# Optimization experiments

Hardware: AMD Instinct MI355X
Metric: run time of the kernel (lower is better)

The kernel has to match this reference:

```python
import jax, jax.numpy as jnp
import numpy as np

BASE_ALPHA = 0.05
NUM_ITER = 2
EPS = 1e-06


def setup_inputs() -> dict:
    key = jax.random.key(0)
    k1, k2 = jax.random.split(key)
    pred = jax.random.normal(k1, (8, 8192, 3), dtype=jnp.float32)
    partial = jax.random.normal(k2, (8, 2048, 3), dtype=jnp.float32)
    return {"pred": pred, "partial": partial}


def _cdist(a, b):
    # Euclidean pairwise distances via ||a||^2 - 2ab + ||b||^2 (avoids [B,N,M,3] temp).
    a2 = jnp.sum(a * a, axis=-1)  # [B,N]
    b2 = jnp.sum(b * b, axis=-1)  # [B,M]
    d2 = a2[:, :, None] - 2.0 * jnp.einsum('bnd,bmd->bnm', a, b) + b2[:, None, :]
    return jnp.sqrt(jnp.maximum(d2, 0.0))


def reference(pred, partial):
    refined = pred
    for _ in range(NUM_ITER):
        dist = _cdist(refined, partial)          # [B,N,M]
        min_dist = jnp.min(dist, axis=-1)        # [B,N]
        min_idx = jnp.argmin(dist, axis=-1)      # [B,N]
        nearest = jnp.take_along_axis(partial, min_idx[:, :, None], axis=1)  # [B,N,3]
        dist_norm = min_dist / (jnp.max(min_dist, axis=-1, keepdims=True) + EPS)
        alpha = BASE_ALPHA * (2.0 - dist_norm)   # [B,N]
        refined = refined + alpha[:, :, None] * (nearest - refined)
    return refined
```

## Files before the change

### kernel.cpp

```cpp
#include <hip/hip_runtime.h>
#include <math.h>

#define BATCH 8
#define NPRED 8192
#define MPART 2048
#define NPTS  (BATCH * NPRED)
#define MTOT  (BATCH * MPART)
#define QPL   4
#define SPLIT 16
#define PTS_PER_SPLIT (MPART / SPLIT)
#define GPS   (PTS_PER_SPLIT / 4)
#define QPB   256
#define NBLK  (NPTS / QPB)
#define BLK_PER_B (NPRED / QPB)
#define BASE_ALPHA 0.05f
#define EPS 1e-6f

__global__ __launch_bounds__(256) void prep_kernel(const float* __restrict__ partial,
                                                   float* __restrict__ ppgf,
                                                   float4* __restrict__ near4) {
    const int m = blockIdx.x * 256 + threadIdx.x;
    const float* p = partial + 3u * (unsigned)m;
    const float x = p[0], y = p[1], z = p[2];
    const int g = m >> 2, c = m & 3;
    float* base = ppgf + (size_t)g * 16 + c;
    base[0]  = -2.0f * x;
    base[4]  = -2.0f * y;
    base[8]  = -2.0f * z;
    base[12] = fmaf(x, x, fmaf(y, y, z * z));
    near4[m] = make_float4(x, y, z, 0.0f);
}

template <bool FUSE>
__global__ __launch_bounds__(1024) void nn_kernel(
    const float* __restrict__ src,
    const float4* __restrict__ ppg,
    const float4* __restrict__ near4,
    const float* md_in, const int* idx_in,
    const float* __restrict__ bmax_in,
    float* __restrict__ refined_out,
    float* md_out, int* idx_out,
    float* __restrict__ bmax_out)
{
    __shared__ float4 ldsP[2048];
    __shared__ float smax[4];
    unsigned long long* lk = (unsigned long long*)ldsP;

    const int qb   = blockIdx.x;
    const int b    = qb >> 5;
    const int tid  = threadIdx.x;
    const int wave = tid >> 6, lane = tid & 63;
    const int split = wave;

    const float4* gsrc = ppg + ((size_t)b << 11);
    ldsP[tid]        = gsrc[tid];
    ldsP[tid + 1024] = gsrc[tid + 1024];

    float axq[QPL], ayq[QPL], azq[QPL], a2q[QPL];
    if (FUSE) {
        float v = bmax_in[(b << 5) + (lane & 31)];
        #pragma unroll
        for (int o = 32; o > 0; o >>= 1) v = fmaxf(v, __shfl_down(v, o, 64));
        const float maxv = __shfl(v, 0, 64);
        #pragma unroll
        for (int j = 0; j < QPL; ++j) {
            const int t = (qb << 8) + (j << 6) + lane;
            const float md = md_in[t];
            const int   id = idx_in[t];
            const float alpha = BASE_ALPHA * (2.0f - md / (maxv + EPS));
            const float4 nb = near4[((size_t)b << 11) + id];
            const float* p = src + 3u * (unsigned)t;
            const float px = p[0], py = p[1], pz = p[2];
            axq[j] = fmaf(alpha, nb.x - px, px);
            ayq[j] = fmaf(alpha, nb.y - py, py);
            azq[j] = fmaf(alpha, nb.z - pz, pz);
            if (split == 0) {
                float* o = refined_out + 3u * (unsigned)t;
                o[0] = axq[j]; o[1] = ayq[j]; o[2] = azq[j];
            }
        }
    } else {
        #pragma unroll
        for (int j = 0; j < QPL; ++j) {
            const int t = (qb << 8) + (j << 6) + lane;
            const float* p = src + 3u * (unsigned)t;
            axq[j] = p[0]; ayq[j] = p[1]; azq[j] = p[2];
        }
    }
    #pragma unroll
    for (int j = 0; j < QPL; ++j)
        a2q[j] = fmaf(axq[j], axq[j], fmaf(ayq[j], ayq[j], azq[j] * azq[j]));

    __syncthreads();

    const float4* wp = ldsP + split * (GPS * 4);
    float best[QPL]; int bg[QPL];
    #pragma unroll
    for (int j = 0; j < QPL; ++j) { best[j] = 1e30f; bg[j] = 0; }

    #pragma unroll 2
    for (int i = 0; i < GPS; ++i) {
        const float4 X = wp[4 * i + 0];
        const float4 Y = wp[4 * i + 1];
        const float4 Z = wp[4 * i + 2];
        const float4 W = wp[4 * i + 3];
        #pragma unroll
        for (int j = 0; j < QPL; ++j) {
            const float ax = axq[j], ay = ayq[j], az = azq[j];
            const float d0 = fmaf(Z.x, az, fmaf(Y.x, ay, X.x * ax)) + W.x;
            const float d1 = fmaf(Z.y, az, fmaf(Y.y, ay, X.y * ax)) + W.y;
            const float d2 = fmaf(Z.z, az, fmaf(Y.z, ay, X.z * ax)) + W.z;
            const float d3 = fmaf(Z.w, az, fmaf(Y.w, ay, X.w * ax)) + W.w;
            const float gm = fminf(fminf(fminf(d0, d1), d2), d3);
            if (gm < best[j]) bg[j] = i;
            best[j] = fminf(best[j], gm);
        }
    }

    unsigned long long key[QPL];
    #pragma unroll
    for (int j = 0; j < QPL; ++j) {
        const int gi = bg[j];
        const float4 X = wp[4 * gi + 0];
        const float4 Y = wp[4 * gi + 1];
        const float4 Z = wp[4 * gi + 2];
        const float4 W = wp[4 * gi + 3];
        const float ax = axq[j], ay = ayq[j], az = azq[j];
        const float d0 = fmaf(Z.x, az, fmaf(Y.x, ay, X.x * ax)) + W.x;
        const float d1 = fmaf(Z.y, az, fmaf(Y.y, ay, X.y * ax)) + W.y;
        const float d2 = fmaf(Z.z, az, fmaf(Y.z, ay, X.z * ax)) + W.z;
        const float bv = best[j];
        int c;
        if      (d0 == bv) c = 0;
        else if (d1 == bv) c = 1;
        else if (d2 == bv) c = 2;
        else               c = 3;
        const int m = (split << 7) + (gi << 2) + c;
        const float dd = fmaxf(bv + a2q[j], 0.0f);
        key[j] = ((unsigned long long)__float_as_uint(dd) << 32) | (unsigned)m;
    }

    __syncthreads();
    #pragma unroll
    for (int j = 0; j < QPL; ++j)
        lk[split * QPB + (j << 6) + lane] = key[j];
    __syncthreads();

    if (wave < 4) {
        const int q2 = (wave << 6) + lane;
        unsigned long long kk = lk[q2];
        #pragma unroll
        for (int s = 1; s < SPLIT; ++s) {
            const unsigned long long k = lk[s * QPB + q2];
            if (k < kk) kk = k;
        }
        const float md = sqrtf(__uint_as_float((unsigned)(kk >> 32)));
        const int t2 = (qb << 8) + q2;
        md_out[t2]  = md;
        idx_out[t2] = (int)(kk & 0xffffffffu);
        float w = md;
        #pragma unroll
        for (int o = 32; o > 0; o >>= 1) w = fmaxf(w, __shfl_down(w, o, 64));
        if (lane == 0) smax[wave] = w;
    }
    __syncthreads();
    if (tid == 0)
        bmax_out[qb] = fmaxf(fmaxf(smax[0], smax[1]), fmaxf(smax[2], smax[3]));
}

__global__ __launch_bounds__(256) void update_kernel(
    const float* __restrict__ refined1,
    const float4* __restrict__ near4,
    const float* __restrict__ md2,
    const int*   __restrict__ idx2,
    const float* __restrict__ bmax2,
    float* __restrict__ out)
{
    const int t = blockIdx.x * 256 + threadIdx.x;
    const int b = t >> 13;
    const int lane = threadIdx.x & 63;
    float v = bmax2[(b << 5) + (lane & 31)];
    #pragma unroll
    for (int o = 32; o > 0; o >>= 1) v = fmaxf(v, __shfl_down(v, o, 64));
    const float maxv = __shfl(v, 0, 64);
    const float md = md2[t];
    const int   id = idx2[t];
    const float alpha = BASE_ALPHA * (2.0f - md / (maxv + EPS));
    const float4 nb = near4[((size_t)b << 11) + id];
    const float* p = refined1 + 3u * (unsigned)t;
    const float px = p[0], py = p[1], pz = p[2];
    float* o = out + 3u * (unsigned)t;
    o[0] = fmaf(alpha, nb.x - px, px);
    o[1] = fmaf(alpha, nb.y - py, py);
    o[2] = fmaf(alpha, nb.z - pz, pz);
}

extern "C" void kernel_launch(void* const* d_in, const int* in_sizes, int n_in,
                              void* d_out, int out_size, void* d_ws, size_t ws_size,
                              hipStream_t stream) {
    const float* pred    = (const float*)d_in[0];
    const float* partial = (const float*)d_in[1];
    float* out = (float*)d_out;

    char* ws = (char*)d_ws;
    float4* ppg   = (float4*)ws;
    float4* near4 = (float4*)(ws + 262144);
    float*  ref1  = (float*)(ws + 524288);
    float*  md1   = (float*)(ws + 1310720);
    int*    idx1  = (int*)(ws + 1572864);
    float*  bmax1 = (float*)(ws + 1835008);
    float*  bmax2 = bmax1 + NBLK;

    prep_kernel<<<MTOT / 256, 256, 0, stream>>>(partial, (float*)ppg, near4);

    nn_kernel<false><<<NBLK, 1024, 0, stream>>>(
        pred, ppg, near4, nullptr, nullptr, nullptr, nullptr, md1, idx1, bmax1);

    nn_kernel<true><<<NBLK, 1024, 0, stream>>>(
        pred, ppg, near4, md1, idx1, bmax1, ref1, md1, idx1, bmax2);

    update_kernel<<<NPTS / 256, 256, 0, stream>>>(ref1, near4, md1, idx1, bmax2, out);
}
```

Measured before the change: 98.96 us.

## Stream partial-point groups via scalar loads instead of LDS staging

The inner nearest-neighbour loop now reads each group of four precomputed partial points straight from global memory with inline s_load_dwordx16 into scalar registers, using a wave-uniform split index. This drops the LDS staging copy, the barrier that followed it, and the per-lane LDS reads. Each iteration waits on lgkmcnt(0) before computing, so scalar load latency is exposed with little overlap. The final re-check now reads the winning group from global memory.

```diff
diff --git a/kernel.cpp b/kernel.cpp
--- a/kernel.cpp
+++ b/kernel.cpp
@@ -16,6 +16,8 @@
 #define BASE_ALPHA 0.05f
 #define EPS 1e-6f
 
+typedef float fx16 __attribute__((ext_vector_type(16)));
+
 __global__ __launch_bounds__(256) void prep_kernel(const float* __restrict__ partial,
                                                    float* __restrict__ ppgf,
                                                    float4* __restrict__ near4) {
@@ -42,19 +44,14 @@
     float* md_out, int* idx_out,
     float* __restrict__ bmax_out)
 {
-    __shared__ float4 ldsP[2048];
+    __shared__ unsigned long long lk[SPLIT * QPB];
     __shared__ float smax[4];
-    unsigned long long* lk = (unsigned long long*)ldsP;
 
     const int qb   = blockIdx.x;
     const int b    = qb >> 5;
     const int tid  = threadIdx.x;
     const int wave = tid >> 6, lane = tid & 63;
-    const int split = wave;
-
-    const float4* gsrc = ppg + ((size_t)b << 11);
-    ldsP[tid]        = gsrc[tid];
-    ldsP[tid + 1024] = gsrc[tid + 1024];
+    const int split = __builtin_amdgcn_readfirstlane(wave);
 
     float axq[QPL], ayq[QPL], azq[QPL], a2q[QPL];
     if (FUSE) {
@@ -91,40 +88,54 @@
     for (int j = 0; j < QPL; ++j)
         a2q[j] = fmaf(axq[j], axq[j], fmaf(ayq[j], ayq[j], azq[j] * azq[j]));
 
-    __syncthreads();
-
-    const float4* wp = ldsP + split * (GPS * 4);
+    const fx16* gq = (const fx16*)(ppg + ((size_t)b << 11) + ((size_t)split << 7));
+
     float best[QPL]; int bg[QPL];
     #pragma unroll
     for (int j = 0; j < QPL; ++j) { best[j] = 1e30f; bg[j] = 0; }
 
-    #pragma unroll 2
-    for (int i = 0; i < GPS; ++i) {
-        const float4 X = wp[4 * i + 0];
-        const float4 Y = wp[4 * i + 1];
-        const float4 Z = wp[4 * i + 2];
-        const float4 W = wp[4 * i + 3];
+    #pragma unroll 1
+    for (int ii = 0; ii < GPS; ii += 2) {
+        fx16 A, B;
+        asm volatile("s_load_dwordx16 %0, %2, 0\n\t"
+                     "s_load_dwordx16 %1, %2, 64"
+                     : "=&s"(A), "=&s"(B)
+                     : "s"(gq + ii));
+        asm volatile("s_waitcnt lgkmcnt(0)" : "+s"(A), "+s"(B));
+
         #pragma unroll
         for (int j = 0; j < QPL; ++j) {
             const float ax = axq[j], ay = ayq[j], az = azq[j];
-            const float d0 = fmaf(Z.x, az, fmaf(Y.x, ay, X.x * ax)) + W.x;
-            const float d1 = fmaf(Z.y, az, fmaf(Y.y, ay, X.y * ax)) + W.y;
-            const float d2 = fmaf(Z.z, az, fmaf(Y.z, ay, X.z * ax)) + W.z;
-            const float d3 = fmaf(Z.w, az, fmaf(Y.w, ay, X.w * ax)) + W.w;
+            const float d0 = fmaf(A[8],  az, fmaf(A[4], ay, A[0] * ax)) + A[12];
+            const float d1 = fmaf(A[9],  az, fmaf(A[5], ay, A[1] * ax)) + A[13];
+            const float d2 = fmaf(A[10], az, fmaf(A[6], ay, A[2] * ax)) + A[14];
+            const float d3 = fmaf(A[11], az, fmaf(A[7], ay, A[3] * ax)) + A[15];
             const float gm = fminf(fminf(fminf(d0, d1), d2), d3);
-            if (gm < best[j]) bg[j] = i;
+            if (gm < best[j]) bg[j] = ii;
             best[j] = fminf(best[j], gm);
         }
-    }
-
+        #pragma unroll
+        for (int j = 0; j < QPL; ++j) {
+            const float ax = axq[j], ay = ayq[j], az = azq[j];
+            const float d0 = fmaf(B[8],  az, fmaf(B[4], ay, B[0] * ax)) + B[12];
+            const float d1 = fmaf(B[9],  az, fmaf(B[5], ay, B[1] * ax)) + B[13];
+            const float d2 = fmaf(B[10], az, fmaf(B[6], ay, B[2] * ax)) + B[14];
+            const float d3 = fmaf(B[11], az, fmaf(B[7], ay, B[3] * ax)) + B[15];
+            const float gm = fminf(fminf(fminf(d0, d1), d2), d3);
+            if (gm < best[j]) bg[j] = ii + 1;
+            best[j] = fminf(best[j], gm);
+        }
+    }
+
+    const float4* wpg = ppg + ((size_t)b << 11) + ((size_t)split << 7);
     unsigned long long key[QPL];
     #pragma unroll
     for (int j = 0; j < QPL; ++j) {
         const int gi = bg[j];
-        const float4 X = wp[4 * gi + 0];
-        const float4 Y = wp[4 * gi + 1];
-        const float4 Z = wp[4 * gi + 2];
-        const float4 W = wp[4 * gi + 3];
+        const float4 X = wpg[4 * gi + 0];
+        const float4 Y = wpg[4 * gi + 1];
+        const float4 Z = wpg[4 * gi + 2];
+        const float4 W = wpg[4 * gi + 3];
         const float ax = axq[j], ay = ayq[j], az = azq[j];
         const float d0 = fmaf(Z.x, az, fmaf(Y.x, ay, X.x * ax)) + W.x;
         const float d1 = fmaf(Z.y, az, fmaf(Y.y, ay, X.y * ax)) + W.y;
@@ -140,7 +151,6 @@
         key[j] = ((unsigned long long)__float_as_uint(dd) << 32) | (unsigned)m;
     }
 
-    __syncthreads();
     #pragma unroll
     for (int j = 0; j < QPL; ++j)
         lk[split * QPB + (j << 6) + lane] = key[j];
```

Result: slower. 108.7 us (+9.8%).

## Fuse all passes into one cooperative kernel with grid syncs

Applied to the files above, without the earlier changes.

Replaces the prep, two nearest-neighbour passes and the update kernel with a single cooperative kernel. Each block builds its batch's partial-point tile in LDS, and grid.sync is used to exchange the per-block distance maxima between iterations. Per-point state (refined coordinates, min distance, index) stays in registers and LDS instead of round-tripping through global memory, and three launches disappear. The cost is two grid-wide barriers and the requirement that all 256 blocks of 1024 threads be co-resident, which depends on the device's CU count and the larger LDS footprint per block.

```diff
diff --git a/kernel.cpp b/kernel.cpp
--- a/kernel.cpp
+++ b/kernel.cpp
@@ -1,99 +1,36 @@
 #include <hip/hip_runtime.h>
+#include <hip/hip_cooperative_groups.h>
 #include <math.h>
+
+namespace cg = cooperative_groups;
 
 #define BATCH 8
 #define NPRED 8192
 #define MPART 2048
 #define NPTS  (BATCH * NPRED)
-#define MTOT  (BATCH * MPART)
 #define QPL   4
 #define SPLIT 16
 #define PTS_PER_SPLIT (MPART / SPLIT)
 #define GPS   (PTS_PER_SPLIT / 4)
 #define QPB   256
 #define NBLK  (NPTS / QPB)
-#define BLK_PER_B (NPRED / QPB)
 #define BASE_ALPHA 0.05f
 #define EPS 1e-6f
 
-__global__ __launch_bounds__(256) void prep_kernel(const float* __restrict__ partial,
-                                                   float* __restrict__ ppgf,
-                                                   float4* __restrict__ near4) {
-    const int m = blockIdx.x * 256 + threadIdx.x;
-    const float* p = partial + 3u * (unsigned)m;
-    const float x = p[0], y = p[1], z = p[2];
-    const int g = m >> 2, c = m & 3;
-    float* base = ppgf + (size_t)g * 16 + c;
-    base[0]  = -2.0f * x;
-    base[4]  = -2.0f * y;
-    base[8]  = -2.0f * z;
-    base[12] = fmaf(x, x, fmaf(y, y, z * z));
-    near4[m] = make_float4(x, y, z, 0.0f);
-}
-
-template <bool FUSE>
-__global__ __launch_bounds__(1024) void nn_kernel(
-    const float* __restrict__ src,
-    const float4* __restrict__ ppg,
-    const float4* __restrict__ near4,
-    const float* md_in, const int* idx_in,
-    const float* __restrict__ bmax_in,
-    float* __restrict__ refined_out,
-    float* md_out, int* idx_out,
-    float* __restrict__ bmax_out)
+struct SMem {
+    float4 tileP[2048];
+    unsigned long long lk[SPLIT * QPB];
+    float md_s[QPB];
+    int   idx_s[QPB];
+    float smax[4];
+};
+
+__device__ __forceinline__ void nn_pass(
+    SMem& sm, int qb, int tid, int wave, int lane, int split,
+    const float axq[QPL], const float ayq[QPL], const float azq[QPL],
+    const float a2q[QPL], float* __restrict__ bmax_entry)
 {
-    __shared__ float4 ldsP[2048];
-    __shared__ float smax[4];
-    unsigned long long* lk = (unsigned long long*)ldsP;
-
-    const int qb   = blockIdx.x;
-    const int b    = qb >> 5;
-    const int tid  = threadIdx.x;
-    const int wave = tid >> 6, lane = tid & 63;
-    const int split = wave;
-
-    const float4* gsrc = ppg + ((size_t)b << 11);
-    ldsP[tid]        = gsrc[tid];
-    ldsP[tid + 1024] = gsrc[tid + 1024];
-
-    float axq[QPL], ayq[QPL], azq[QPL], a2q[QPL];
-    if (FUSE) {
-        float v = bmax_in[(b << 5) + (lane & 31)];
-        #pragma unroll
-        for (int o = 32; o > 0; o >>= 1) v = fmaxf(v, __shfl_down(v, o, 64));
-        const float maxv = __shfl(v, 0, 64);
-        #pragma unroll
-        for (int j = 0; j < QPL; ++j) {
-            const int t = (qb << 8) + (j << 6) + lane;
-            const float md = md_in[t];
-            const int   id = idx_in[t];
-            const float alpha = BASE_ALPHA * (2.0f - md / (maxv + EPS));
-            const float4 nb = near4[((size_t)b << 11) + id];
-            const float* p = src + 3u * (unsigned)t;
-            const float px = p[0], py = p[1], pz = p[2];
-            axq[j] = fmaf(alpha, nb.x - px, px);
-            ayq[j] = fmaf(alpha, nb.y - py, py);
-            azq[j] = fmaf(alpha, nb.z - pz, pz);
-            if (split == 0) {
-                float* o = refined_out + 3u * (unsigned)t;
-                o[0] = axq[j]; o[1] = ayq[j]; o[2] = azq[j];
-            }
-        }
-    } else {
-        #pragma unroll
-        for (int j = 0; j < QPL; ++j) {
-            const int t = (qb << 8) + (j << 6) + lane;
-            const float* p = src + 3u * (unsigned)t;
-            axq[j] = p[0]; ayq[j] = p[1]; azq[j] = p[2];
-        }
-    }
-    #pragma unroll
-    for (int j = 0; j < QPL; ++j)
-        a2q[j] = fmaf(axq[j], axq[j], fmaf(ayq[j], ayq[j], azq[j] * azq[j]));
-
-    __syncthreads();
-
-    const float4* wp = ldsP + split * (GPS * 4);
+    const float4* wp = sm.tileP + split * (GPS * 4);
     float best[QPL]; int bg[QPL];
     #pragma unroll
     for (int j = 0; j < QPL; ++j) { best[j] = 1e30f; bg[j] = 0; }
@@ -143,56 +80,138 @@
     __syncthreads();
     #pragma unroll
     for (int j = 0; j < QPL; ++j)
-        lk[split * QPB + (j << 6) + lane] = key[j];
+        sm.lk[split * QPB + (j << 6) + lane] = key[j];
     __syncthreads();
 
     if (wave < 4) {
         const int q2 = (wave << 6) + lane;
-        unsigned long long kk = lk[q2];
+        unsigned long long kk = sm.lk[q2];
         #pragma unroll
         for (int s = 1; s < SPLIT; ++s) {
-            const unsigned long long k = lk[s * QPB + q2];
+            const unsigned long long k = sm.lk[s * QPB + q2];
             if (k < kk) kk = k;
         }
         const float md = sqrtf(__uint_as_float((unsigned)(kk >> 32)));
-        const int t2 = (qb << 8) + q2;
-        md_out[t2]  = md;
-        idx_out[t2] = (int)(kk & 0xffffffffu);
+        sm.md_s[q2]  = md;
+        sm.idx_s[q2] = (int)(kk & 0xffffffffu);
         float w = md;
         #pragma unroll
         for (int o = 32; o > 0; o >>= 1) w = fmaxf(w, __shfl_down(w, o, 64));
-        if (lane == 0) smax[wave] = w;
+        if (lane == 0) sm.smax[wave] = w;
     }
     __syncthreads();
     if (tid == 0)
-        bmax_out[qb] = fmaxf(fmaxf(smax[0], smax[1]), fmaxf(smax[2], smax[3]));
+        *bmax_entry = fmaxf(fmaxf(sm.smax[0], sm.smax[1]),
+                            fmaxf(sm.smax[2], sm.smax[3]));
 }
 
-__global__ __launch_bounds__(256) void update_kernel(
-    const float* __restrict__ refined1,
-    const float4* __restrict__ near4,
-    const float* __restrict__ md2,
-    const int*   __restrict__ idx2,
-    const float* __restrict__ bmax2,
-    float* __restrict__ out)
+__global__ void __launch_bounds__(1024) fused_kernel(
+    const float* __restrict__ pred,
+    const float* __restrict__ partial,
+    float* __restrict__ out,
+    float* __restrict__ bmax1,
+    float* __restrict__ bmax2)
 {
-    const int t = blockIdx.x * 256 + threadIdx.x;
-    const int b = t >> 13;
-    const int lane = threadIdx.x & 63;
-    float v = bmax2[(b << 5) + (lane & 31)];
+    __shared__ SMem sm;
+    cg::grid_group grid = cg::this_grid();
+
+    const int qb   = blockIdx.x;
+    const int b    = qb >> 5;
+    const int tid  = threadIdx.x;
+    const int wave = tid >> 6, lane = tid & 63;
+    const int split = wave;
+
+    float axq[QPL], ayq[QPL], azq[QPL], a2q[QPL];
+    #pragma unroll
+    for (int j = 0; j < QPL; ++j) {
+        const int t = (qb << 8) + (j << 6) + lane;
+        const float* p = pred + 3u * (unsigned)t;
+        axq[j] = p[0]; ayq[j] = p[1]; azq[j] = p[2];
+    }
+    #pragma unroll
+    for (int j = 0; j < QPL; ++j)
+        a2q[j] = fmaf(axq[j], axq[j], fmaf(ayq[j], ayq[j], azq[j] * azq[j]));
+
+    {
+        float4* raws = (float4*)sm.lk;
+        const float4* psrc = (const float4*)(partial + (size_t)b * MPART * 3);
+        raws[tid] = psrc[tid];
+        if (tid < 512) raws[tid + 1024] = psrc[tid + 1024];
+    }
+    __syncthreads();
+
+    {
+        const float* rf = (const float*)sm.lk;
+        float* tpf = (float*)sm.tileP;
+        #pragma unroll
+        for (int k = 0; k < 2; ++k) {
+            const int m = tid + k * 1024;
+            const float x = rf[3 * m], y = rf[3 * m + 1], z = rf[3 * m + 2];
+            const int g = m >> 2, c = m & 3;
+            float* basep = tpf + g * 16 + c;
+            basep[0]  = -2.0f * x;
+            basep[4]  = -2.0f * y;
+            basep[8]  = -2.0f * z;
+            basep[12] = fmaf(x, x, fmaf(y, y, z * z));
+        }
+    }
+    __syncthreads();
+
+    nn_pass(sm, qb, tid, wave, lane, split, axq, ayq, azq, a2q, bmax1 + qb);
+    __threadfence();
+    grid.sync();
+
+    float v = bmax1[(b << 5) + (lane & 31)];
     #pragma unroll
     for (int o = 32; o > 0; o >>= 1) v = fmaxf(v, __shfl_down(v, o, 64));
-    const float maxv = __shfl(v, 0, 64);
-    const float md = md2[t];
-    const int   id = idx2[t];
-    const float alpha = BASE_ALPHA * (2.0f - md / (maxv + EPS));
-    const float4 nb = near4[((size_t)b << 11) + id];
-    const float* p = refined1 + 3u * (unsigned)t;
-    const float px = p[0], py = p[1], pz = p[2];
-    float* o = out + 3u * (unsigned)t;
-    o[0] = fmaf(alpha, nb.x - px, px);
-    o[1] = fmaf(alpha, nb.y - py, py);
-    o[2] = fmaf(alpha, nb.z - pz, pz);
+    const float maxv1 = __shfl(v, 0, 64);
+
+    const float* tpf = (const float*)sm.tileP;
+    #pragma unroll
+    for (int j = 0; j < QPL; ++j) {
+        const int q = (j << 6) + lane;
+        const float md = sm.md_s[q];
+        const int  id  = sm.idx_s[q];
+        const float alpha = BASE_ALPHA * (2.0f - md / (maxv1 + EPS));
+        const int g = id >> 2, c = id & 3;
+        const float nbx = -0.5f * tpf[g * 16 + c];
+        const float nby = -0.5f * tpf[g * 16 + 4 + c];
+        const float nbz = -0.5f * tpf[g * 16 + 8 + c];
+        const float px = axq[j], py = ayq[j], pz = azq[j];
+        axq[j] = fmaf(alpha, nbx - px, px);
+        ayq[j] = fmaf(alpha, nby - py, py);
+        azq[j] = fmaf(alpha, nbz - pz, pz);
+    }
+    #pragma unroll
+    for (int j = 0; j < QPL; ++j)
+        a2q[j] = fmaf(axq[j], axq[j], fmaf(ayq[j], ayq[j], azq[j] * azq[j]));
+
+    nn_pass(sm, qb, tid, wave, lane, split, axq, ayq, azq, a2q, bmax2 + qb);
+    __threadfence();
+    grid.sync();
+
+    float v2 = bmax2[(b << 5) + (lane & 31)];
+    #pragma unroll
+    for (int o = 32; o > 0; o >>= 1) v2 = fmaxf(v2, __shfl_down(v2, o, 64));
+    const float maxv2 = __shfl(v2, 0, 64);
+
+    if (wave < 4) {
+        const int j = wave;
+        const int q = (j << 6) + lane;
+        const float md = sm.md_s[q];
+        const int  id  = sm.idx_s[q];
+        const float alpha = BASE_ALPHA * (2.0f - md / (maxv2 + EPS));
+        const int g = id >> 2, c = id & 3;
+        const float nbx = -0.5f * tpf[g * 16 + c];
+        const float nby = -0.5f * tpf[g * 16 + 4 + c];
+        const float nbz = -0.5f * tpf[g * 16 + 8 + c];
+        const float px = axq[j], py = ayq[j], pz = azq[j];
+        const int t = (qb << 8) + q;
+        float* o = out + 3u * (unsigned)t;
+        o[0] = fmaf(alpha, nbx - px, px);
+        o[1] = fmaf(alpha, nby - py, py);
+        o[2] = fmaf(alpha, nbz - pz, pz);
+    }
 }
 
 extern "C" void kernel_launch(void* const* d_in, const int* in_sizes, int n_in,
@@ -203,21 +222,11 @@
     float* out = (float*)d_out;
 
     char* ws = (char*)d_ws;
-    float4* ppg   = (float4*)ws;
-    float4* near4 = (float4*)(ws + 262144);
-    float*  ref1  = (float*)(ws + 524288);
-    float*  md1   = (float*)(ws + 1310720);
-    int*    idx1  = (int*)(ws + 1572864);
-    float*  bmax1 = (float*)(ws + 1835008);
-    float*  bmax2 = bmax1 + NBLK;
-
-    prep_kernel<<<MTOT / 256, 256, 0, stream>>>(partial, (float*)ppg, near4);
-
-    nn_kernel<false><<<NBLK, 1024, 0, stream>>>(
-        pred, ppg, near4, nullptr, nullptr, nullptr, nullptr, md1, idx1, bmax1);
-
-    nn_kernel<true><<<NBLK, 1024, 0, stream>>>(
-        pred, ppg, near4, md1, idx1, bmax1, ref1, md1, idx1, bmax2);
-
-    update_kernel<<<NPTS / 256, 256, 0, stream>>>(ref1, near4, md1, idx1, bmax2, out);
+    float* bmax1 = (float*)ws;
+    float* bmax2 = bmax1 + NBLK;
+
+    void* args[] = {(void*)&pred, (void*)&partial, (void*)&out,
+                    (void*)&bmax1, (void*)&bmax2};
+    hipLaunchCooperativeKernel((const void*)fused_kernel,
+                               dim3(NBLK), dim3(1024), args, 0, stream);
 }
```

Measured after the change: 274.0 us. 2.77x slower.

## Fuse partial-cloud preprocessing into NN kernel and software-pipeline LDS loads

Applied to the files above, without the earlier changes.

Drops the separate prep kernel. Each NN block now loads the raw partial points into shared memory and builds the SoA (-2x, -2y, -2z, |p|^2) tile itself, and nearest-neighbour coordinates are read back from that tile or from the raw partial array. The inner distance loop is software-pipelined, prefetching the next group's LDS values, and the final reduction over splits now uses all 16 waves with cross-lane xor shuffles instead of 4 waves doing serial loops. This saves one launch and the global round trip for the preprocessed data, in exchange for redundant per-block preprocessing, more LDS use (extra key buffer) and possible register pressure.

```diff
diff --git a/kernel.cpp b/kernel.cpp
--- a/kernel.cpp
+++ b/kernel.cpp
@@ -5,46 +5,35 @@
 #define NPRED 8192
 #define MPART 2048
 #define NPTS  (BATCH * NPRED)
-#define MTOT  (BATCH * MPART)
 #define QPL   4
 #define SPLIT 16
 #define PTS_PER_SPLIT (MPART / SPLIT)
 #define GPS   (PTS_PER_SPLIT / 4)
 #define QPB   256
 #define NBLK  (NPTS / QPB)
-#define BLK_PER_B (NPRED / QPB)
 #define BASE_ALPHA 0.05f
 #define EPS 1e-6f
 
-__global__ __launch_bounds__(256) void prep_kernel(const float* __restrict__ partial,
-                                                   float* __restrict__ ppgf,
-                                                   float4* __restrict__ near4) {
-    const int m = blockIdx.x * 256 + threadIdx.x;
-    const float* p = partial + 3u * (unsigned)m;
-    const float x = p[0], y = p[1], z = p[2];
-    const int g = m >> 2, c = m & 3;
-    float* base = ppgf + (size_t)g * 16 + c;
-    base[0]  = -2.0f * x;
-    base[4]  = -2.0f * y;
-    base[8]  = -2.0f * z;
-    base[12] = fmaf(x, x, fmaf(y, y, z * z));
-    near4[m] = make_float4(x, y, z, 0.0f);
+__device__ __forceinline__ unsigned long long shflx_u64(unsigned long long v, int m) {
+    unsigned lo = (unsigned)v, hi = (unsigned)(v >> 32);
+    lo = (unsigned)__shfl_xor((int)lo, m, 64);
+    hi = (unsigned)__shfl_xor((int)hi, m, 64);
+    return ((unsigned long long)hi << 32) | lo;
 }
 
 template <bool FUSE>
 __global__ __launch_bounds__(1024) void nn_kernel(
     const float* __restrict__ src,
-    const float4* __restrict__ ppg,
-    const float4* __restrict__ near4,
+    const float* __restrict__ partial,
     const float* md_in, const int* idx_in,
     const float* __restrict__ bmax_in,
     float* __restrict__ refined_out,
     float* md_out, int* idx_out,
     float* __restrict__ bmax_out)
 {
-    __shared__ float4 ldsP[2048];
-    __shared__ float smax[4];
-    unsigned long long* lk = (unsigned long long*)ldsP;
+    __shared__ float4 tileP[2048];
+    __shared__ unsigned long long lk[SPLIT * QPB];
+    __shared__ float smax[SPLIT];
 
     const int qb   = blockIdx.x;
     const int b    = qb >> 5;
@@ -52,11 +41,15 @@
     const int wave = tid >> 6, lane = tid & 63;
     const int split = wave;
 
-    const float4* gsrc = ppg + ((size_t)b << 11);
-    ldsP[tid]        = gsrc[tid];
-    ldsP[tid + 1024] = gsrc[tid + 1024];
+    {
+        float4* raws = (float4*)lk;
+        const float4* psrc = (const float4*)(partial + (size_t)b * MPART * 3);
+        raws[tid] = psrc[tid];
+        if (tid < 512) raws[tid + 1024] = psrc[tid + 1024];
+    }
 
     float axq[QPL], ayq[QPL], azq[QPL], a2q[QPL];
+    float alpha_[QPL]; int id_[QPL];
     if (FUSE) {
         float v = bmax_in[(b << 5) + (lane & 31)];
         #pragma unroll
@@ -66,44 +59,69 @@
         for (int j = 0; j < QPL; ++j) {
             const int t = (qb << 8) + (j << 6) + lane;
             const float md = md_in[t];
-            const int   id = idx_in[t];
-            const float alpha = BASE_ALPHA * (2.0f - md / (maxv + EPS));
-            const float4 nb = near4[((size_t)b << 11) + id];
+            id_[j]    = idx_in[t];
+            alpha_[j] = BASE_ALPHA * (2.0f - md / (maxv + EPS));
             const float* p = src + 3u * (unsigned)t;
-            const float px = p[0], py = p[1], pz = p[2];
-            axq[j] = fmaf(alpha, nb.x - px, px);
-            ayq[j] = fmaf(alpha, nb.y - py, py);
-            azq[j] = fmaf(alpha, nb.z - pz, pz);
+            axq[j] = p[0]; ayq[j] = p[1]; azq[j] = p[2];
+        }
+    } else {
+        #pragma unroll
+        for (int j = 0; j < QPL; ++j) {
+            const int t = (qb << 8) + (j << 6) + lane;
+            const float* p = src + 3u * (unsigned)t;
+            axq[j] = p[0]; ayq[j] = p[1]; azq[j] = p[2];
+        }
+    }
+
+    __syncthreads();
+
+    {
+        const float* rf = (const float*)lk;
+        float* tpf = (float*)tileP;
+        #pragma unroll
+        for (int k = 0; k < 2; ++k) {
+            const int m = tid + (k << 10);
+            const float x = rf[3 * m], y = rf[3 * m + 1], z = rf[3 * m + 2];
+            const int g = m >> 2, c = m & 3;
+            float* basep = tpf + g * 16 + c;
+            basep[0]  = -2.0f * x;
+            basep[4]  = -2.0f * y;
+            basep[8]  = -2.0f * z;
+            basep[12] = fmaf(x, x, fmaf(y, y, z * z));
+        }
+    }
+    __syncthreads();
+
+    const float* tpf = (const float*)tileP;
+    if (FUSE) {
+        #pragma unroll
+        for (int j = 0; j < QPL; ++j) {
+            const int g = id_[j] >> 2, c = id_[j] & 3;
+            const float nbx = -0.5f * tpf[g * 16 + c];
+            const float nby = -0.5f * tpf[g * 16 + 4 + c];
+            const float nbz = -0.5f * tpf[g * 16 + 8 + c];
+            const float px = axq[j], py = ayq[j], pz = azq[j];
+            axq[j] = fmaf(alpha_[j], nbx - px, px);
+            ayq[j] = fmaf(alpha_[j], nby - py, py);
+            azq[j] = fmaf(alpha_[j], nbz - pz, pz);
             if (split == 0) {
+                const int t = (qb << 8) + (j << 6) + lane;
                 float* o = refined_out + 3u * (unsigned)t;
                 o[0] = axq[j]; o[1] = ayq[j]; o[2] = azq[j];
             }
         }
-    } else {
-        #pragma unroll
-        for (int j = 0; j < QPL; ++j) {
-            const int t = (qb << 8) + (j << 6) + lane;
-            const float* p = src + 3u * (unsigned)t;
-            axq[j] = p[0]; ayq[j] = p[1]; azq[j] = p[2];
-        }
     }
     #pragma unroll
     for (int j = 0; j < QPL; ++j)
         a2q[j] = fmaf(axq[j], axq[j], fmaf(ayq[j], ayq[j], azq[j] * azq[j]));
 
-    __syncthreads();
-
-    const float4* wp = ldsP + split * (GPS * 4);
+    const float4* wp = tileP + split * (GPS * 4);
     float best[QPL]; int bg[QPL];
     #pragma unroll
     for (int j = 0; j < QPL; ++j) { best[j] = 1e30f; bg[j] = 0; }
 
-    #pragma unroll 2
-    for (int i = 0; i < GPS; ++i) {
-        const float4 X = wp[4 * i + 0];
-        const float4 Y = wp[4 * i + 1];
-        const float4 Z = wp[4 * i + 2];
-        const float4 W = wp[4 * i + 3];
+    auto step = [&](int i, const float4& X, const float4& Y,
+                    const float4& Z, const float4& W) {
         #pragma unroll
         for (int j = 0; j < QPL; ++j) {
             const float ax = axq[j], ay = ayq[j], az = azq[j];
@@ -115,7 +133,19 @@
             if (gm < best[j]) bg[j] = i;
             best[j] = fminf(best[j], gm);
         }
-    }
+    };
+
+    float4 Xc = wp[0], Yc = wp[1], Zc = wp[2], Wc = wp[3];
+    #pragma unroll 4
+    for (int i = 0; i < GPS - 1; ++i) {
+        const float4 Xn = wp[4 * i + 4];
+        const float4 Yn = wp[4 * i + 5];
+        const float4 Zn = wp[4 * i + 6];
+        const float4 Wn = wp[4 * i + 7];
+        step(i, Xc, Yc, Zc, Wc);
+        Xc = Xn; Yc = Yn; Zc = Zn; Wc = Wn;
+    }
+    step(GPS - 1, Xc, Yc, Zc, Wc);
 
     unsigned long long key[QPL];
     #pragma unroll
@@ -140,37 +170,47 @@
         key[j] = ((unsigned long long)__float_as_uint(dd) << 32) | (unsigned)m;
     }
 
-    __syncthreads();
     #pragma unroll
     for (int j = 0; j < QPL; ++j)
         lk[split * QPB + (j << 6) + lane] = key[j];
     __syncthreads();
 
-    if (wave < 4) {
-        const int q2 = (wave << 6) + lane;
-        unsigned long long kk = lk[q2];
-        #pragma unroll
-        for (int s = 1; s < SPLIT; ++s) {
-            const unsigned long long k = lk[s * QPB + q2];
+    {
+        const int q  = (wave << 4) + (lane & 15);
+        const int s0 = (lane >> 4) << 2;
+        unsigned long long kk = lk[s0 * QPB + q];
+        #pragma unroll
+        for (int s = 1; s < 4; ++s) {
+            const unsigned long long k = lk[(s0 + s) * QPB + q];
             if (k < kk) kk = k;
         }
+        unsigned long long o = shflx_u64(kk, 16);
+        if (o < kk) kk = o;
+        o = shflx_u64(kk, 32);
+        if (o < kk) kk = o;
         const float md = sqrtf(__uint_as_float((unsigned)(kk >> 32)));
-        const int t2 = (qb << 8) + q2;
-        md_out[t2]  = md;
-        idx_out[t2] = (int)(kk & 0xffffffffu);
+        if (lane < 16) {
+            const int t2 = (qb << 8) + q;
+            md_out[t2]  = md;
+            idx_out[t2] = (int)(kk & 0xffffffffu);
+        }
         float w = md;
         #pragma unroll
-        for (int o = 32; o > 0; o >>= 1) w = fmaxf(w, __shfl_down(w, o, 64));
+        for (int o2 = 8; o2 > 0; o2 >>= 1) w = fmaxf(w, __shfl_xor(w, o2, 64));
         if (lane == 0) smax[wave] = w;
     }
     __syncthreads();
-    if (tid == 0)
-        bmax_out[qb] = fmaxf(fmaxf(smax[0], smax[1]), fmaxf(smax[2], smax[3]));
+    if (tid == 0) {
+        float m0 = smax[0];
+        #pragma unroll
+        for (int s = 1; s < SPLIT; ++s) m0 = fmaxf(m0, smax[s]);
+        bmax_out[qb] = m0;
+    }
 }
 
 __global__ __launch_bounds__(256) void update_kernel(
     const float* __restrict__ refined1,
-    const float4* __restrict__ near4,
+    const float* __restrict__ partial,
     const float* __restrict__ md2,
     const int*   __restrict__ idx2,
     const float* __restrict__ bmax2,
@@ -186,13 +226,14 @@
     const float md = md2[t];
     const int   id = idx2[t];
     const float alpha = BASE_ALPHA * (2.0f - md / (maxv + EPS));
-    const float4 nb = near4[((size_t)b << 11) + id];
+    const float* nbp = partial + 3u * (unsigned)((b << 11) + id);
+    const float nbx = nbp[0], nby = nbp[1], nbz = nbp[2];
     const float* p = refined1 + 3u * (unsigned)t;
     const float px = p[0], py = p[1], pz = p[2];
     float* o = out + 3u * (unsigned)t;
-    o[0] = fmaf(alpha, nb.x - px, px);
-    o[1] = fmaf(alpha, nb.y - py, py);
-    o[2] = fmaf(alpha, nb.z - pz, pz);
+    o[0] = fmaf(alpha, nbx - px, px);
+    o[1] = fmaf(alpha, nby - py, py);
+    o[2] = fmaf(alpha, nbz - pz, pz);
 }
 
 extern "C" void kernel_launch(void* const* d_in, const int* in_sizes, int n_in,
@@ -203,21 +244,17 @@
     float* out = (float*)d_out;
 
     char* ws = (char*)d_ws;
-    float4* ppg   = (float4*)ws;
-    float4* near4 = (float4*)(ws + 262144);
-    float*  ref1  = (float*)(ws + 524288);
-    float*  md1   = (float*)(ws + 1310720);
-    int*    idx1  = (int*)(ws + 1572864);
-    float*  bmax1 = (float*)(ws + 1835008);
-    float*  bmax2 = bmax1 + NBLK;
-
-    prep_kernel<<<MTOT / 256, 256, 0, stream>>>(partial, (float*)ppg, near4);
+    float* ref1  = (float*)ws;
+    float* md1   = (float*)(ws + 786432);
+    int*   idx1  = (int*)(ws + 1048576);
+    float* bmax1 = (float*)(ws + 1310720);
+    float* bmax2 = bmax1 + NBLK;
 
     nn_kernel<false><<<NBLK, 1024, 0, stream>>>(
-        pred, ppg, near4, nullptr, nullptr, nullptr, nullptr, md1, idx1, bmax1);
+        pred, partial, nullptr, nullptr, nullptr, nullptr, md1, idx1, bmax1);
 
     nn_kernel<true><<<NBLK, 1024, 0, stream>>>(
-        pred, ppg, near4, md1, idx1, bmax1, ref1, md1, idx1, bmax2);
-
-    update_kernel<<<NPTS / 256, 256, 0, stream>>>(ref1, near4, md1, idx1, bmax2, out);
-}
+        pred, partial, md1, idx1, bmax1, ref1, md1, idx1, bmax2);
+
+    update_kernel<<<NPTS / 256, 256, 0, stream>>>(ref1, partial, md1, idx1, bmax2, out);
+}
```

Measured after the change: 95.86 us. 1.03x faster.
